# Performance work log

Hardware: AMD Instinct MI355X
Metric: run time of the kernel (lower is better)

Reference implementation:

```python
import jax, jax.numpy as jnp
import numpy as np

D_K = 64
NEG = -1e9


def setup_inputs() -> dict:
    key = jax.random.key(0)
    ks = jax.random.split(key, 7)
    B, N, D = 4, 2048, 1024
    H, dk, dv = 16, 64, 64
    return {
        "q": jax.random.normal(ks[0], (B, N, D), dtype=jnp.float32),
        "k": jax.random.normal(ks[1], (B, N, D), dtype=jnp.float32),
        "v": jax.random.normal(ks[2], (B, N, D), dtype=jnp.float32),
        "w_q": jax.random.normal(ks[3], (H, D, dk), dtype=jnp.float32),
        "w_k": jax.random.normal(ks[4], (H, D, dk), dtype=jnp.float32),
        "w_v": jax.random.normal(ks[5], (H, D, dv), dtype=jnp.float32),
        "w_o": jax.random.normal(ks[6], (H * dv, D), dtype=jnp.float32),
    }


def reference(q, k, v, w_q, w_k, w_v, w_o):
    B, n, d_model = q.shape
    H = w_q.shape[0]
    dv = w_v.shape[-1]
    # per-head projections: [B,H,n,dk]
    qh = jnp.einsum('bnd,hdk->bhnk', q, w_q)
    kh = jnp.einsum('bnd,hdk->bhnk', k, w_k)
    vh = jnp.einsum('bnd,hdk->bhnk', v, w_v)
    logits = jnp.einsum('bhqk,bhsk->bhqs', qh, kh) / jnp.sqrt(jnp.float32(D_K))
    causal = jnp.tril(jnp.ones((n, n), dtype=bool))
    logits = jnp.where(causal[None, None], logits, jnp.float32(NEG))
    attn = jax.nn.softmax(logits, axis=-1)
    o = jnp.einsum('bhqs,bhsv->bhqv', attn, vh)       # [B,H,n,dv]
    o = o.transpose(0, 2, 1, 3).reshape(B, n, H * dv)  # [B,n,H*dv]
    return o @ w_o
```

## Files before the change

### kernel.cpp

```cpp
#include <hip/hip_runtime.h>


typedef short bf16;
typedef short bf16x8 __attribute__((ext_vector_type(8)));
typedef float f32x4  __attribute__((ext_vector_type(4)));

constexpr int B_ = 4, N_ = 2048, D_ = 1024, H_ = 16, DK_ = 64;

static __device__ __forceinline__ bf16 f2bf(float f) {
    union { float f; unsigned u; } x; x.f = f;
    const unsigned r = x.u + 0x7FFFu + ((x.u >> 16) & 1u);
    return (bf16)(r >> 16);
}
static __device__ __forceinline__ float bf2f(bf16 s) {
    union { unsigned u; float f; } x; x.u = ((unsigned)(unsigned short)s) << 16;
    return x.f;
}
static __device__ __forceinline__ f32x4 mfma16(bf16x8 a, bf16x8 b, f32x4 c) {
    return __builtin_amdgcn_mfma_f32_16x16x32_bf16(a, b, c, 0, 0, 0);
}
template <int CTRL>
static __device__ __forceinline__ float dpp_mov(float x) {
    return __int_as_float(__builtin_amdgcn_update_dpp(
        __float_as_int(x), __float_as_int(x), CTRL, 0xF, 0xF, false));
}
static __device__ __forceinline__ float rowmax16(float x) {
    x = fmaxf(x, dpp_mov<0x128>(x));
    x = fmaxf(x, dpp_mov<0x124>(x));
    x = fmaxf(x, dpp_mov<0x122>(x));
    x = fmaxf(x, dpp_mov<0x121>(x));
    return x;
}
static __device__ __forceinline__ void gload16(const bf16* g, bf16* lds) {
    __builtin_amdgcn_global_load_lds(
        (const __attribute__((address_space(1))) void*)g,
        (__attribute__((address_space(3))) void*)lds, 16, 0, 0);
}


__global__ __launch_bounds__(256) void prep_kernel(
    const float* __restrict__ v,  const float* __restrict__ wq,
    const float* __restrict__ wk, const float* __restrict__ wv,
    const float* __restrict__ wo,
    bf16* __restrict__ v_t,
    bf16* __restrict__ wq_t_hi, bf16* __restrict__ wq_t_lo,
    bf16* __restrict__ wk_t_hi, bf16* __restrict__ wk_t_lo,
    bf16* __restrict__ wv_t, bf16* __restrict__ wo_t) {
    const int sec  = blockIdx.y;
    const int tid  = blockIdx.x * blockDim.x + threadIdx.x;
    const int nthr = gridDim.x * blockDim.x;
    if (sec == 0) {
        const int n8 = (B_ * N_ * D_) / 8;
        for (int i8 = tid; i8 < n8; i8 += nthr) {
            const size_t o = (size_t)i8 * 8;
            const int e   = (int)(o & 4095);
            const int kkt = (int)((o >> 12) & 15);
            const int st  = (int)((o >> 16) & 31);
            const int b   = (int)(o >> 21);
            const int ks = e >> 11, f = (e >> 9) & 3, lg = (e >> 7) & 3, lr = (e >> 3) & 15;
            const int s = st * 64 + f * 16 + lr;
            const int d = kkt * 64 + ks * 32 + lg * 8;
            const float4* sp = reinterpret_cast<const float4*>(
                v + ((size_t)(b * N_ + s)) * D_ + d);
            const float4 f0 = sp[0], f1 = sp[1];
            const float ff[8] = {f0.x, f0.y, f0.z, f0.w, f1.x, f1.y, f1.z, f1.w};
            bf16x8 o8;
#pragma unroll
            for (int j = 0; j < 8; ++j) o8[j] = f2bf(ff[j]);
            *reinterpret_cast<bf16x8*>(v_t + o) = o8;
        }
    } else if (sec == 1 || sec == 2) {
        const float* w = (sec == 1) ? wq : wk;
        bf16* whi = (sec == 1) ? wq_t_hi : wk_t_hi;
        bf16* wlo = (sec == 1) ? wq_t_lo : wk_t_lo;
        const int n8 = (H_ * DK_ * D_) / 8;
        for (int i8 = tid; i8 < n8; i8 += nthr) {
            const int o = i8 * 8;
            const int e = o & 4095, kkt = (o >> 12) & 15, h = o >> 16;
            const int ks = e >> 11, f = (e >> 9) & 3, lg = (e >> 7) & 3, lr = (e >> 3) & 15;
            const int c  = f * 16 + lr;
            const int kg = kkt * 64 + ks * 32 + lg * 8;
            bf16x8 h8, l8;
#pragma unroll
            for (int j = 0; j < 8; ++j) {
                const float fv = w[((size_t)h * D_ + kg + j) * DK_ + c];
                const bf16 hi = f2bf(fv);
                h8[j] = hi;
                l8[j] = f2bf(fv - bf2f(hi));
            }
            *reinterpret_cast<bf16x8*>(whi + o) = h8;
            *reinterpret_cast<bf16x8*>(wlo + o) = l8;
        }
    } else if (sec == 3) {
        const int n8 = (H_ * DK_ * D_) / 8;
        for (int i8 = tid; i8 < n8; i8 += nthr) {
            const int o = i8 * 8;
            const int e = o & 4095, kkt = (o >> 12) & 15, h = o >> 16;
            const int ks = e >> 11, f = (e >> 9) & 3, lg = (e >> 7) & 3, lr = (e >> 3) & 15;
            const int d  = f * 16 + lr;
            const int kg = kkt * 64 + ks * 32 + lg * 8;
            bf16x8 o8;
#pragma unroll
            for (int j = 0; j < 8; ++j)
                o8[j] = f2bf(wv[((size_t)h * D_ + kg + j) * DK_ + d]);
            *reinterpret_cast<bf16x8*>(wv_t + o) = o8;
        }
    } else {
        const int n8 = (D_ * D_) / 8;
        for (int i8 = tid; i8 < n8; i8 += nthr) {
            const int o = i8 * 8;
            const int e = o & 4095, kkt = (o >> 12) & 15, cg = o >> 16;
            const int ks = e >> 11, f = (e >> 9) & 3, lg = (e >> 7) & 3, lr = (e >> 3) & 15;
            const int c  = cg * 64 + f * 16 + lr;
            const int kg = kkt * 64 + ks * 32 + lg * 8;
            bf16x8 o8;
#pragma unroll
            for (int j = 0; j < 8; ++j)
                o8[j] = f2bf(wo[(size_t)(kg + j) * D_ + c]);
            *reinterpret_cast<bf16x8*>(wo_t + o) = o8;
        }
    }
}

__global__ __launch_bounds__(256, 2) void proj_qk_kernel(
    const float* __restrict__ q, const float* __restrict__ k,
    const bf16* __restrict__ wq_t_hi, const bf16* __restrict__ wq_t_lo,
    const bf16* __restrict__ wk_t_hi, const bf16* __restrict__ wk_t_lo,
    bf16* __restrict__ qh_hi, bf16* __restrict__ qh_lo,
    bf16* __restrict__ kh_t_hi, bf16* __restrict__ kh_t_lo) {
    __shared__ __align__(16) unsigned char alds[32768];
    const int mat = blockIdx.y >> 2;
    const int cg  = blockIdx.y & 3;
    const float* x    = mat ? k : q;
    const bf16* wT_hi = mat ? wk_t_hi : wq_t_hi;
    const bf16* wT_lo = mat ? wk_t_lo : wq_t_lo;
    const float scale = mat ? 1.0f : 0.125f;

    const int m0 = blockIdx.x * 128;
    const int t  = threadIdx.x;
    const int w  = t >> 6;
    const int l  = t & 63;
    const int lr = l & 15, lg = l >> 4;
    const int srow = t >> 3;
    const int scol = (t & 7) * 8;
    const int h = cg * 4 + w;

    f32x4 acc[8][4] = {};
    for (int kk = 0; kk < D_; kk += 64) {
        float4 st[4][2];
#pragma unroll
        for (int it = 0; it < 4; ++it) {
            const float4* ap = reinterpret_cast<const float4*>(
                x + (size_t)(m0 + srow + it * 32) * D_ + kk + scol);
            st[it][0] = ap[0]; st[it][1] = ap[1];
        }
        __syncthreads();
#pragma unroll
        for (int it = 0; it < 4; ++it) {
            const int r = srow + it * 32;
            const float ff[8] = {st[it][0].x, st[it][0].y, st[it][0].z, st[it][0].w,
                                 st[it][1].x, st[it][1].y, st[it][1].z, st[it][1].w};
            bf16x8 hi8, lo8;
#pragma unroll
            for (int j = 0; j < 8; ++j) {
                const float f   = ff[j] * scale;
                const bf16 hiv = f2bf(f);
                hi8[j] = hiv;
                lo8[j] = f2bf(f - bf2f(hiv));
            }
            const int byte = r * 128 + ((scol * 2) ^ ((r & 7) << 4));
            *reinterpret_cast<bf16x8*>(alds + byte)         = hi8;
            *reinterpret_cast<bf16x8*>(alds + 16384 + byte) = lo8;
        }
        __syncthreads();
        const int kkt = kk >> 6;
#pragma unroll
        for (int ks = 0; ks < 2; ++ks) {
            bf16x8 a_hi[8], a_lo[8];
#pragma unroll
            for (int mf = 0; mf < 8; ++mf) {
                const int row  = mf * 16 + lr;
                const int byte = row * 128 + ((ks * 64 + lg * 16) ^ ((row & 7) << 4));
                a_hi[mf] = *reinterpret_cast<const bf16x8*>(alds + byte);
                a_lo[mf] = *reinterpret_cast<const bf16x8*>(alds + 16384 + byte);
            }
#pragma unroll
            for (int nf = 0; nf < 4; ++nf) {
                const size_t boff = ((size_t)(h * 16 + kkt)) * 4096 +
                                    ks * 2048 + nf * 512 + lg * 128 + lr * 8;
                const bf16x8 b_hi = *reinterpret_cast<const bf16x8*>(wT_hi + boff);
                const bf16x8 b_lo = *reinterpret_cast<const bf16x8*>(wT_lo + boff);
#pragma unroll
                for (int mf = 0; mf < 8; ++mf) {
                    acc[mf][nf] = mfma16(a_hi[mf], b_hi, acc[mf][nf]);
                    acc[mf][nf] = mfma16(a_hi[mf], b_lo, acc[mf][nf]);
                    acc[mf][nf] = mfma16(a_lo[mf], b_hi, acc[mf][nf]);
                }
            }
        }
    }
#pragma unroll
    for (int mf = 0; mf < 8; ++mf)
#pragma unroll
        for (int nf = 0; nf < 4; ++nf)
#pragma unroll
            for (int i = 0; i < 4; ++i) {
                const int m = m0 + mf * 16 + lg * 4 + i;
                const int b = m >> 11, n = m & (N_ - 1);
                const float val = acc[mf][nf][i];
                const bf16 hi = f2bf(val);
                const bf16 lo = f2bf(val - bf2f(hi));
                if (mat == 0) {
                    const int c = nf * 16 + lr;
                    const size_t oidx = (((size_t)(b * H_ + h)) * N_ + n) * DK_ + c;
                    qh_hi[oidx] = hi;
                    qh_lo[oidx] = lo;
                } else {
                    const size_t oidx =
                        ((size_t)(b * H_ + h) * 32 + (n >> 6)) * 4096 +
                        (nf >> 1) * 2048 + (mf & 3) * 512 +
                        (((nf << 1) + (lr >> 3)) & 3) * 128 +
                        (lg * 4 + i) * 8 + (lr & 7);
                    kh_t_hi[oidx] = hi;
                    kh_t_lo[oidx] = lo;
                }
            }
}

__global__ __launch_bounds__(256) void proj_v_kernel(
    const bf16* __restrict__ v_t, const bf16* __restrict__ wv_t,
    bf16* __restrict__ vh_t) {
    const int bh = blockIdx.y;
    const int b = bh >> 4, h = bh & 15;
    const int st = blockIdx.x;
    const int w = threadIdx.x >> 6, l = threadIdx.x & 63;
    const int lr = l & 15, lg = l >> 4;

    f32x4 acc[4] = {};
    for (int kk = 0; kk < D_; kk += 32) {
        const int kkt = kk >> 6, ks = (kk >> 5) & 1;
        const bf16x8 a = *reinterpret_cast<const bf16x8*>(
            wv_t + ((size_t)(h * 16 + kkt)) * 4096 + ks * 2048 + w * 512 + lg * 128 + lr * 8);
#pragma unroll
        for (int nf = 0; nf < 4; ++nf) {
            const bf16x8 bb = *reinterpret_cast<const bf16x8*>(
                v_t + ((size_t)((b * 32 + st) * 16 + kkt)) * 4096 +
                ks * 2048 + nf * 512 + lg * 128 + lr * 8);
            acc[nf] = mfma16(a, bb, acc[nf]);
        }
    }
#pragma unroll
    for (int nf = 0; nf < 4; ++nf)
#pragma unroll
        for (int i = 0; i < 4; ++i) {
            const size_t oidx =
                ((size_t)(b * H_ + h) * 32 + st) * 4096 +
                (nf >> 1) * 2048 + w * 512 +
                (((nf << 1) + (lr >> 3)) & 3) * 128 +
                (lg * 4 + i) * 8 + (lr & 7);
            vh_t[oidx] = f2bf(acc[nf][i]);
        }
}

static __device__ __forceinline__ void stage_tile(
    const bf16* khh, const bf16* khl, const bf16* vht,
    bf16* buf, int st, int w, int l) {
    const bf16* kh = khh + (size_t)st * 4096;
    const bf16* kl = khl + (size_t)st * 4096;
    const bf16* vv = vht + (size_t)st * 4096;
#pragma unroll
    for (int i = 0; i < 6; ++i) {
        const int c = w * 6 + i;
        const bf16* src = (c < 8) ? kh + c * 512
                        : (c < 16) ? kl + (c - 8) * 512
                                   : vv + (c - 16) * 512;
        gload16(src + l * 8, buf + c * 512);
    }
}

__global__ __launch_bounds__(256, 2) void attn_kernel(
    const bf16* __restrict__ qh_hi, const bf16* __restrict__ qh_lo,
    const bf16* __restrict__ kh_t_hi, const bf16* __restrict__ kh_t_lo,
    const bf16* __restrict__ vh_t, bf16* __restrict__ o_flat) {
    __shared__ __align__(16) bf16 lds[2 * 12288 + 4 * 1024];
    const int bid  = blockIdx.x;
    const int wgid = (bid & 7) * 64 + (bid >> 3);
    const int bh   = wgid >> 3;
    const int p8   = wgid & 7;
    const int b = bh >> 4, h = bh & 15;
    const int w = threadIdx.x >> 6, l = threadIdx.x & 63;
    const int lr = l & 15, lg = l >> 4;
    unsigned char* myp = (unsigned char*)(lds + 24576 + w * 1024);
    const size_t hb = (size_t)(b * H_ + h);
    const bf16* khh = kh_t_hi + hb * 32 * 4096;
    const bf16* khl = kh_t_lo + hb * 32 * 4096;
    const bf16* vht = vh_t    + hb * 32 * 4096;

    bf16x8 ones;
#pragma unroll
    for (int j = 0; j < 8; ++j) ones[j] = (bf16)0x3F80;

    for (int phase = 0; phase < 4; ++phase) {
        const int qt = (phase == 0) ? p8 : (phase == 1) ? 31 - p8
                     : (phase == 2) ? p8 + 8 : 23 - p8;
        const int q0 = qt * 64 + w * 16;

        bf16x8 qf_hi[2], qf_lo[2];
#pragma unroll
        for (int ks = 0; ks < 2; ++ks) {
            const size_t off = (hb * N_ + q0 + lr) * DK_ + ks * 32 + lg * 8;
            qf_hi[ks] = *reinterpret_cast<const bf16x8*>(qh_hi + off);
            qf_lo[ks] = *reinterpret_cast<const bf16x8*>(qh_lo + off);
        }

        f32x4 m_run, l_acc, o_acc[4];
#pragma unroll
        for (int i = 0; i < 4; ++i) { m_run[i] = -3e38f; l_acc[i] = 0.f; }
#pragma unroll
        for (int dt = 0; dt < 4; ++dt) o_acc[dt] = f32x4{0.f, 0.f, 0.f, 0.f};

        const int nt = qt + 1;
        stage_tile(khh, khl, vht, lds, 0, w, l);
        for (int t = 0; t < nt; ++t) {
            bf16* cur = lds + (t & 1) * 12288;
            bf16* nxt = lds + ((t + 1) & 1) * 12288;
            if (t + 1 < nt) {
                stage_tile(khh, khl, vht, nxt, t + 1, w, l);
                asm volatile("s_waitcnt vmcnt(6)" ::: "memory");
            } else {
                asm volatile("s_waitcnt vmcnt(0)" ::: "memory");
            }
            __builtin_amdgcn_s_barrier();
            const int s0 = t * 64;
            f32x4 sacc[4];
#pragma unroll
            for (int f = 0; f < 4; ++f) {
                sacc[f] = f32x4{0.f, 0.f, 0.f, 0.f};
#pragma unroll
                for (int ks = 0; ks < 2; ++ks) {
                    const bf16x8 khi = *reinterpret_cast<const bf16x8*>(
                        cur + ks * 2048 + f * 512 + l * 8);
                    const bf16x8 klo = *reinterpret_cast<const bf16x8*>(
                        cur + 4096 + ks * 2048 + f * 512 + l * 8);
                    sacc[f] = mfma16(qf_hi[ks], khi, sacc[f]);
                    sacc[f] = mfma16(qf_hi[ks], klo, sacc[f]);
                    sacc[f] = mfma16(qf_lo[ks], khi, sacc[f]);
                }
            }
            if (t == nt - 1) {
#pragma unroll
                for (int f = 0; f < 4; ++f) {
                    const int s = s0 + f * 16 + lr;
#pragma unroll
                    for (int i = 0; i < 4; ++i) {
                        const int qq = q0 + lg * 4 + i;
                        if (s > qq) sacc[f][i] = -1e9f;
                    }
                }
            }
            f32x4 m_new, escale;
#pragma unroll
            for (int i = 0; i < 4; ++i) {
                float tm = fmaxf(fmaxf(sacc[0][i], sacc[1][i]),
                                 fmaxf(sacc[2][i], sacc[3][i]));
                tm = rowmax16(tm);
                m_new[i]  = fmaxf(m_run[i], tm);
                escale[i] = __expf(m_run[i] - m_new[i]);
                m_run[i]  = m_new[i];
            }
#pragma unroll
            for (int f = 0; f < 4; ++f)
#pragma unroll
                for (int i = 0; i < 4; ++i) {
                    const float p = __expf(sacc[f][i] - m_new[i]);
                    const int row = lg * 4 + i, col = f * 16 + lr;
                    const int byte = (row * 128 + col * 2) ^ ((row & 7) << 4);
                    *reinterpret_cast<bf16*>(myp + byte) = f2bf(p);
                }
#pragma unroll
            for (int i = 0; i < 4; ++i) l_acc[i] *= escale[i];
#pragma unroll
            for (int dt = 0; dt < 4; ++dt)
#pragma unroll
                for (int i = 0; i < 4; ++i) o_acc[dt][i] *= escale[i];
            bf16x8 pa[2];
#pragma unroll
            for (int ks = 0; ks < 2; ++ks) {
                const int byte = (lr * 128 + ks * 64 + lg * 16) ^ ((lr & 7) << 4);
                pa[ks] = *reinterpret_cast<const bf16x8*>(myp + byte);
            }
#pragma unroll
            for (int dt = 0; dt < 4; ++dt)
#pragma unroll
                for (int ks = 0; ks < 2; ++ks) {
                    const bf16x8 vb = *reinterpret_cast<const bf16x8*>(
                        cur + 8192 + ks * 2048 + dt * 512 + l * 8);
                    o_acc[dt] = mfma16(pa[ks], vb, o_acc[dt]);
                }
#pragma unroll
            for (int ks = 0; ks < 2; ++ks)
                l_acc = mfma16(pa[ks], ones, l_acc);
            asm volatile("s_waitcnt lgkmcnt(0)" ::: "memory");
            __builtin_amdgcn_s_barrier();
        }
#pragma unroll
        for (int dt = 0; dt < 4; ++dt)
#pragma unroll
            for (int i = 0; i < 4; ++i) {
                const int qq = q0 + lg * 4 + i;
                const float val = o_acc[dt][i] / l_acc[i];
                o_flat[((size_t)b * N_ + qq) * (H_ * DK_) + h * DK_ + dt * 16 + lr] =
                    f2bf(val);
            }
    }
}

__global__ __launch_bounds__(256, 4) void outproj_kernel(
    const bf16* __restrict__ o_flat, const bf16* __restrict__ wo_t,
    float* __restrict__ out) {
    __shared__ __align__(16) unsigned char alds[16384];
    const int m0 = blockIdx.x * 128;
    const int cg = blockIdx.y;
    const int t = threadIdx.x;
    const int w = t >> 6, l = t & 63;
    const int lr = l & 15, lg = l >> 4;
    const int srow = t >> 3;
    const int scb  = (t & 7) * 16;

    f32x4 acc[2][4] = {};
    for (int kk = 0; kk < D_; kk += 64) {
        bf16x8 st[4];
#pragma unroll
        for (int it = 0; it < 4; ++it)
            st[it] = *reinterpret_cast<const bf16x8*>(
                o_flat + (size_t)(m0 + srow + it * 32) * D_ + kk + (t & 7) * 8);
        __syncthreads();
#pragma unroll
        for (int it = 0; it < 4; ++it) {
            const int r = srow + it * 32;
            *reinterpret_cast<bf16x8*>(alds + r * 128 + (scb ^ ((r & 7) << 4))) = st[it];
        }
        __syncthreads();
        const int kkt = kk >> 6;
#pragma unroll
        for (int ks = 0; ks < 2; ++ks) {
            bf16x8 a[2];
#pragma unroll
            for (int mf = 0; mf < 2; ++mf) {
                const int row = w * 32 + mf * 16 + lr;
                a[mf] = *reinterpret_cast<const bf16x8*>(
                    alds + row * 128 + ((ks * 64 + lg * 16) ^ ((row & 7) << 4)));
            }
#pragma unroll
            for (int nf = 0; nf < 4; ++nf) {
                const bf16x8 bb = *reinterpret_cast<const bf16x8*>(
                    wo_t + ((size_t)(cg * 16 + kkt)) * 4096 +
                    ks * 2048 + nf * 512 + lg * 128 + lr * 8);
#pragma unroll
                for (int mf = 0; mf < 2; ++mf)
                    acc[mf][nf] = mfma16(a[mf], bb, acc[mf][nf]);
            }
        }
    }
#pragma unroll
    for (int mf = 0; mf < 2; ++mf)
#pragma unroll
        for (int nf = 0; nf < 4; ++nf)
#pragma unroll
            for (int i = 0; i < 4; ++i) {
                const int m = m0 + w * 32 + mf * 16 + lg * 4 + i;
                out[(size_t)m * D_ + cg * 64 + nf * 16 + lr] = acc[mf][nf][i];
            }
}

extern "C" void kernel_launch(void* const* d_in, const int* in_sizes, int n_in,
                              void* d_out, int out_size, void* d_ws, size_t ws_size,
                              hipStream_t stream) {
    const float* q  = (const float*)d_in[0];
    const float* k  = (const float*)d_in[1];
    const float* v  = (const float*)d_in[2];
    const float* wq = (const float*)d_in[3];
    const float* wk = (const float*)d_in[4];
    const float* wv = (const float*)d_in[5];
    const float* wo = (const float*)d_in[6];
    float* out = (float*)d_out;

    char* p = (char*)d_ws;
    auto alloc = [&](size_t elems) {
        bf16* r = (bf16*)p;
        p += ((elems * 2 + 255) / 256) * 256;
        return r;
    };
    bf16* v_t     = alloc((size_t)B_ * N_ * D_);
    bf16* wq_t_hi = alloc((size_t)H_ * DK_ * D_);
    bf16* wq_t_lo = alloc((size_t)H_ * DK_ * D_);
    bf16* wk_t_hi = alloc((size_t)H_ * DK_ * D_);
    bf16* wk_t_lo = alloc((size_t)H_ * DK_ * D_);
    bf16* wv_t    = alloc((size_t)H_ * DK_ * D_);
    bf16* wo_t    = alloc((size_t)D_ * D_);
    bf16* qh_hi   = alloc((size_t)B_ * H_ * N_ * DK_);
    bf16* qh_lo   = alloc((size_t)B_ * H_ * N_ * DK_);
    bf16* kh_t_hi = alloc((size_t)B_ * H_ * N_ * DK_);
    bf16* kh_t_lo = alloc((size_t)B_ * H_ * N_ * DK_);
    bf16* vh_t    = alloc((size_t)B_ * H_ * DK_ * N_);
    bf16* o_flat  = alloc((size_t)B_ * N_ * H_ * DK_);

    if ((size_t)(p - (char*)d_ws) > ws_size) return;

    prep_kernel<<<dim3(1024, 5), 256, 0, stream>>>(v, wq, wk, wv, wo, v_t,
                                                   wq_t_hi, wq_t_lo, wk_t_hi, wk_t_lo,
                                                   wv_t, wo_t);
    proj_qk_kernel<<<dim3(64, 8), 256, 0, stream>>>(q, k, wq_t_hi, wq_t_lo,
                                                    wk_t_hi, wk_t_lo,
                                                    qh_hi, qh_lo, kh_t_hi, kh_t_lo);
    proj_v_kernel<<<dim3(32, 64), 256, 0, stream>>>(v_t, wv_t, vh_t);
    attn_kernel<<<512, 256, 0, stream>>>(qh_hi, qh_lo, kh_t_hi, kh_t_lo, vh_t, o_flat);
    outproj_kernel<<<dim3(64, 16), 256, 0, stream>>>(o_flat, wo_t, out);
}
```

Baseline: 467.9 us.

## Enlarge attention query tile to 128 rows and widen out-projection tile

The attention kernel now gives each workgroup 128-row query bands (32 rows per wave, two MFMA row fragments), so each staged K/V tile feeds twice as many queries. The phase loop drops from four 64-row tiles to two 128-row bands, and waves skip K tiles that lie entirely above their causal limit. The out-projection kernel doubles its column tile per block to 128, which halves the grid and reuses A-tile loads across more columns. These raise register use and reduce the number of blocks, which may lower occupancy and worsen load balance.

```diff
diff --git a/kernel.cpp b/kernel.cpp
--- a/kernel.cpp
+++ b/kernel.cpp
@@ -36,7 +36,6 @@
         (const __attribute__((address_space(1))) void*)g,
         (__attribute__((address_space(3))) void*)lds, 16, 0, 0);
 }
-
 
 __global__ __launch_bounds__(256) void prep_kernel(
     const float* __restrict__ v,  const float* __restrict__ wq,
@@ -282,7 +281,7 @@
     const bf16* __restrict__ qh_hi, const bf16* __restrict__ qh_lo,
     const bf16* __restrict__ kh_t_hi, const bf16* __restrict__ kh_t_lo,
     const bf16* __restrict__ vh_t, bf16* __restrict__ o_flat) {
-    __shared__ __align__(16) bf16 lds[2 * 12288 + 4 * 1024];
+    __shared__ __align__(16) bf16 lds[2 * 12288 + 4 * 2048];
     const int bid  = blockIdx.x;
     const int wgid = (bid & 7) * 64 + (bid >> 3);
     const int bh   = wgid >> 3;
@@ -290,7 +289,7 @@
     const int b = bh >> 4, h = bh & 15;
     const int w = threadIdx.x >> 6, l = threadIdx.x & 63;
     const int lr = l & 15, lg = l >> 4;
-    unsigned char* myp = (unsigned char*)(lds + 24576 + w * 1024);
+    unsigned char* myp = (unsigned char*)(lds + 24576 + w * 2048);
     const size_t hb = (size_t)(b * H_ + h);
     const bf16* khh = kh_t_hi + hb * 32 * 4096;
     const bf16* khl = kh_t_lo + hb * 32 * 4096;
@@ -300,26 +299,30 @@
 #pragma unroll
     for (int j = 0; j < 8; ++j) ones[j] = (bf16)0x3F80;
 
-    for (int phase = 0; phase < 4; ++phase) {
-        const int qt = (phase == 0) ? p8 : (phase == 1) ? 31 - p8
-                     : (phase == 2) ? p8 + 8 : 23 - p8;
-        const int q0 = qt * 64 + w * 16;
-
-        bf16x8 qf_hi[2], qf_lo[2];
-#pragma unroll
-        for (int ks = 0; ks < 2; ++ks) {
-            const size_t off = (hb * N_ + q0 + lr) * DK_ + ks * 32 + lg * 8;
-            qf_hi[ks] = *reinterpret_cast<const bf16x8*>(qh_hi + off);
-            qf_lo[ks] = *reinterpret_cast<const bf16x8*>(qh_lo + off);
-        }
-
-        f32x4 m_run, l_acc, o_acc[4];
-#pragma unroll
-        for (int i = 0; i < 4; ++i) { m_run[i] = -3e38f; l_acc[i] = 0.f; }
-#pragma unroll
-        for (int dt = 0; dt < 4; ++dt) o_acc[dt] = f32x4{0.f, 0.f, 0.f, 0.f};
-
-        const int nt = qt + 1;
+    for (int phase = 0; phase < 2; ++phase) {
+        const int band = phase ? (15 - p8) : p8;
+        const int q0 = band * 128 + w * 32;
+
+        bf16x8 qf_hi[2][2], qf_lo[2][2];
+#pragma unroll
+        for (int mf = 0; mf < 2; ++mf)
+#pragma unroll
+            for (int ks = 0; ks < 2; ++ks) {
+                const size_t off = (hb * N_ + q0 + mf * 16 + lr) * DK_ + ks * 32 + lg * 8;
+                qf_hi[mf][ks] = *reinterpret_cast<const bf16x8*>(qh_hi + off);
+                qf_lo[mf][ks] = *reinterpret_cast<const bf16x8*>(qh_lo + off);
+            }
+
+        f32x4 m_run[2], l_acc[2], o_acc[2][4];
+#pragma unroll
+        for (int mf = 0; mf < 2; ++mf) {
+#pragma unroll
+            for (int i = 0; i < 4; ++i) { m_run[mf][i] = -3e38f; l_acc[mf][i] = 0.f; }
+#pragma unroll
+            for (int dt = 0; dt < 4; ++dt) o_acc[mf][dt] = f32x4{0.f, 0.f, 0.f, 0.f};
+        }
+
+        const int nt = 2 * (band + 1);
         stage_tile(khh, khl, vht, lds, 0, w, l);
         for (int t = 0; t < nt; ++t) {
             bf16* cur = lds + (t & 1) * 12288;
@@ -332,86 +335,112 @@
             }
             __builtin_amdgcn_s_barrier();
             const int s0 = t * 64;
-            f32x4 sacc[4];
-#pragma unroll
-            for (int f = 0; f < 4; ++f) {
-                sacc[f] = f32x4{0.f, 0.f, 0.f, 0.f};
-#pragma unroll
-                for (int ks = 0; ks < 2; ++ks) {
-                    const bf16x8 khi = *reinterpret_cast<const bf16x8*>(
-                        cur + ks * 2048 + f * 512 + l * 8);
-                    const bf16x8 klo = *reinterpret_cast<const bf16x8*>(
-                        cur + 4096 + ks * 2048 + f * 512 + l * 8);
-                    sacc[f] = mfma16(qf_hi[ks], khi, sacc[f]);
-                    sacc[f] = mfma16(qf_hi[ks], klo, sacc[f]);
-                    sacc[f] = mfma16(qf_lo[ks], khi, sacc[f]);
+            if (s0 <= q0 + 31) {
+                f32x4 sacc[2][4];
+#pragma unroll
+                for (int mf = 0; mf < 2; ++mf)
+#pragma unroll
+                    for (int f = 0; f < 4; ++f)
+                        sacc[mf][f] = f32x4{0.f, 0.f, 0.f, 0.f};
+#pragma unroll
+                for (int f = 0; f < 4; ++f)
+#pragma unroll
+                    for (int ks = 0; ks < 2; ++ks) {
+                        const bf16x8 khi = *reinterpret_cast<const bf16x8*>(
+                            cur + ks * 2048 + f * 512 + l * 8);
+                        const bf16x8 klo = *reinterpret_cast<const bf16x8*>(
+                            cur + 4096 + ks * 2048 + f * 512 + l * 8);
+#pragma unroll
+                        for (int mf = 0; mf < 2; ++mf) {
+                            sacc[mf][f] = mfma16(qf_hi[mf][ks], khi, sacc[mf][f]);
+                            sacc[mf][f] = mfma16(qf_hi[mf][ks], klo, sacc[mf][f]);
+                            sacc[mf][f] = mfma16(qf_lo[mf][ks], khi, sacc[mf][f]);
+                        }
+                    }
+                if (s0 + 63 > q0) {
+#pragma unroll
+                    for (int mf = 0; mf < 2; ++mf)
+#pragma unroll
+                        for (int f = 0; f < 4; ++f) {
+                            const int s = s0 + f * 16 + lr;
+#pragma unroll
+                            for (int i = 0; i < 4; ++i) {
+                                const int qq = q0 + mf * 16 + lg * 4 + i;
+                                if (s > qq) sacc[mf][f][i] = -1e9f;
+                            }
+                        }
                 }
-            }
-            if (t == nt - 1) {
-#pragma unroll
-                for (int f = 0; f < 4; ++f) {
-                    const int s = s0 + f * 16 + lr;
+                f32x4 escale[2];
+#pragma unroll
+                for (int mf = 0; mf < 2; ++mf)
 #pragma unroll
                     for (int i = 0; i < 4; ++i) {
-                        const int qq = q0 + lg * 4 + i;
-                        if (s > qq) sacc[f][i] = -1e9f;
+                        float tm = fmaxf(fmaxf(sacc[mf][0][i], sacc[mf][1][i]),
+                                         fmaxf(sacc[mf][2][i], sacc[mf][3][i]));
+                        tm = rowmax16(tm);
+                        const float mn = fmaxf(m_run[mf][i], tm);
+                        escale[mf][i] = __expf(m_run[mf][i] - mn);
+                        m_run[mf][i]  = mn;
                     }
+#pragma unroll
+                for (int mf = 0; mf < 2; ++mf)
+#pragma unroll
+                    for (int f = 0; f < 4; ++f)
+#pragma unroll
+                        for (int i = 0; i < 4; ++i) {
+                            const float p = __expf(sacc[mf][f][i] - m_run[mf][i]);
+                            const int row = mf * 16 + lg * 4 + i, col = f * 16 + lr;
+                            const int byte = (row * 128 + col * 2) ^ ((row & 7) << 4);
+                            *reinterpret_cast<bf16*>(myp + byte) = f2bf(p);
+                        }
+#pragma unroll
+                for (int mf = 0; mf < 2; ++mf) {
+#pragma unroll
+                    for (int i = 0; i < 4; ++i) l_acc[mf][i] *= escale[mf][i];
+#pragma unroll
+                    for (int dt = 0; dt < 4; ++dt)
+#pragma unroll
+                        for (int i = 0; i < 4; ++i) o_acc[mf][dt][i] *= escale[mf][i];
                 }
-            }
-            f32x4 m_new, escale;
-#pragma unroll
-            for (int i = 0; i < 4; ++i) {
-                float tm = fmaxf(fmaxf(sacc[0][i], sacc[1][i]),
-                                 fmaxf(sacc[2][i], sacc[3][i]));
-                tm = rowmax16(tm);
-                m_new[i]  = fmaxf(m_run[i], tm);
-                escale[i] = __expf(m_run[i] - m_new[i]);
-                m_run[i]  = m_new[i];
-            }
-#pragma unroll
-            for (int f = 0; f < 4; ++f)
-#pragma unroll
-                for (int i = 0; i < 4; ++i) {
-                    const float p = __expf(sacc[f][i] - m_new[i]);
-                    const int row = lg * 4 + i, col = f * 16 + lr;
-                    const int byte = (row * 128 + col * 2) ^ ((row & 7) << 4);
-                    *reinterpret_cast<bf16*>(myp + byte) = f2bf(p);
-                }
-#pragma unroll
-            for (int i = 0; i < 4; ++i) l_acc[i] *= escale[i];
-#pragma unroll
-            for (int dt = 0; dt < 4; ++dt)
-#pragma unroll
-                for (int i = 0; i < 4; ++i) o_acc[dt][i] *= escale[i];
-            bf16x8 pa[2];
-#pragma unroll
-            for (int ks = 0; ks < 2; ++ks) {
-                const int byte = (lr * 128 + ks * 64 + lg * 16) ^ ((lr & 7) << 4);
-                pa[ks] = *reinterpret_cast<const bf16x8*>(myp + byte);
-            }
-#pragma unroll
-            for (int dt = 0; dt < 4; ++dt)
-#pragma unroll
-                for (int ks = 0; ks < 2; ++ks) {
-                    const bf16x8 vb = *reinterpret_cast<const bf16x8*>(
-                        cur + 8192 + ks * 2048 + dt * 512 + l * 8);
-                    o_acc[dt] = mfma16(pa[ks], vb, o_acc[dt]);
-                }
-#pragma unroll
-            for (int ks = 0; ks < 2; ++ks)
-                l_acc = mfma16(pa[ks], ones, l_acc);
+                bf16x8 pa[2][2];
+#pragma unroll
+                for (int mf = 0; mf < 2; ++mf)
+#pragma unroll
+                    for (int ks = 0; ks < 2; ++ks) {
+                        const int row = mf * 16 + lr;
+                        const int byte = (row * 128 + ks * 64 + lg * 16) ^ ((row & 7) << 4);
+                        pa[mf][ks] = *reinterpret_cast<const bf16x8*>(myp + byte);
+                    }
+#pragma unroll
+                for (int dt = 0; dt < 4; ++dt)
+#pragma unroll
+                    for (int ks = 0; ks < 2; ++ks) {
+                        const bf16x8 vb = *reinterpret_cast<const bf16x8*>(
+                            cur + 8192 + ks * 2048 + dt * 512 + l * 8);
+#pragma unroll
+                        for (int mf = 0; mf < 2; ++mf)
+                            o_acc[mf][dt] = mfma16(pa[mf][ks], vb, o_acc[mf][dt]);
+                    }
+#pragma unroll
+                for (int mf = 0; mf < 2; ++mf)
+#pragma unroll
+                    for (int ks = 0; ks < 2; ++ks)
+                        l_acc[mf] = mfma16(pa[mf][ks], ones, l_acc[mf]);
+            }
             asm volatile("s_waitcnt lgkmcnt(0)" ::: "memory");
             __builtin_amdgcn_s_barrier();
         }
 #pragma unroll
-        for (int dt = 0; dt < 4; ++dt)
-#pragma unroll
-            for (int i = 0; i < 4; ++i) {
-                const int qq = q0 + lg * 4 + i;
-                const float val = o_acc[dt][i] / l_acc[i];
-                o_flat[((size_t)b * N_ + qq) * (H_ * DK_) + h * DK_ + dt * 16 + lr] =
-                    f2bf(val);
-            }
+        for (int mf = 0; mf < 2; ++mf)
+#pragma unroll
+            for (int dt = 0; dt < 4; ++dt)
+#pragma unroll
+                for (int i = 0; i < 4; ++i) {
+                    const int qq = q0 + mf * 16 + lg * 4 + i;
+                    const float val = o_acc[mf][dt][i] / l_acc[mf][i];
+                    o_flat[((size_t)b * N_ + qq) * (H_ * DK_) + h * DK_ + dt * 16 + lr] =
+                        f2bf(val);
+                }
     }
 }
 
@@ -420,14 +449,14 @@
     float* __restrict__ out) {
     __shared__ __align__(16) unsigned char alds[16384];
     const int m0 = blockIdx.x * 128;
-    const int cg = blockIdx.y;
+    const int cp = blockIdx.y;
     const int t = threadIdx.x;
     const int w = t >> 6, l = t & 63;
     const int lr = l & 15, lg = l >> 4;
     const int srow = t >> 3;
     const int scb  = (t & 7) * 16;
 
-    f32x4 acc[2][4] = {};
+    f32x4 acc[2][8] = {};
     for (int kk = 0; kk < D_; kk += 64) {
         bf16x8 st[4];
 #pragma unroll
@@ -452,10 +481,11 @@
                     alds + row * 128 + ((ks * 64 + lg * 16) ^ ((row & 7) << 4)));
             }
 #pragma unroll
-            for (int nf = 0; nf < 4; ++nf) {
+            for (int nf = 0; nf < 8; ++nf) {
+                const int cg = cp * 2 + (nf >> 2);
                 const bf16x8 bb = *reinterpret_cast<const bf16x8*>(
                     wo_t + ((size_t)(cg * 16 + kkt)) * 4096 +
-                    ks * 2048 + nf * 512 + lg * 128 + lr * 8);
+                    ks * 2048 + (nf & 3) * 512 + lg * 128 + lr * 8);
 #pragma unroll
                 for (int mf = 0; mf < 2; ++mf)
                     acc[mf][nf] = mfma16(a[mf], bb, acc[mf][nf]);
@@ -465,11 +495,12 @@
 #pragma unroll
     for (int mf = 0; mf < 2; ++mf)
 #pragma unroll
-        for (int nf = 0; nf < 4; ++nf)
+        for (int nf = 0; nf < 8; ++nf)
 #pragma unroll
             for (int i = 0; i < 4; ++i) {
                 const int m = m0 + w * 32 + mf * 16 + lg * 4 + i;
-                out[(size_t)m * D_ + cg * 64 + nf * 16 + lr] = acc[mf][nf][i];
+                const int c = (cp * 2 + (nf >> 2)) * 64 + (nf & 3) * 16 + lr;
+                out[(size_t)m * D_ + c] = acc[mf][nf][i];
             }
 }
 
@@ -515,5 +546,5 @@
                                                     qh_hi, qh_lo, kh_t_hi, kh_t_lo);
     proj_v_kernel<<<dim3(32, 64), 256, 0, stream>>>(v_t, wv_t, vh_t);
     attn_kernel<<<512, 256, 0, stream>>>(qh_hi, qh_lo, kh_t_hi, kh_t_lo, vh_t, o_flat);
-    outproj_kernel<<<dim3(64, 16), 256, 0, stream>>>(o_flat, wo_t, out);
-}
+    outproj_kernel<<<dim3(64, 8), 256, 0, stream>>>(o_flat, wo_t, out);
+}
```

Measured after the change: 464.4 us. Within noise of the previous version (-0.7%).
